# Performance work log

Measured on AMD Instinct MI355X. Metric: run time of the kernel, lower is better.

## Reference

```python
import jax, jax.numpy as jnp
import numpy as np

B, S, H = 4, 2048, 1024

def setup_inputs() -> dict:
    key = jax.random.key(0)
    ks = jax.random.split(key, 4)
    scale = 1.0 / np.sqrt(H)
    x = jax.random.normal(ks[0], (B, S, H), dtype=jnp.float32)
    Wq = jax.random.normal(ks[1], (H, H), dtype=jnp.float32) * scale
    Wk = jax.random.normal(ks[2], (H, H), dtype=jnp.float32) * scale
    Wv = jax.random.normal(ks[3], (H, H), dtype=jnp.float32) * scale
    bq = jnp.zeros((H,), dtype=jnp.float32)
    bk = jnp.zeros((H,), dtype=jnp.float32)
    bv = jnp.zeros((H,), dtype=jnp.float32)
    return {"x": x, "Wq": Wq, "bq": bq, "Wk": Wk, "bk": bk, "Wv": Wv, "bv": bv}

def reference(x, Wq, bq, Wk, bk, Wv, bv):
    # Linear: y = x @ W^T + b (torch nn.Linear convention)
    Q = jnp.einsum('bsh,oh->bso', x, Wq) + bq
    K = jnp.einsum('bsh,oh->bso', x, Wk) + bk
    V = jnp.einsum('bsh,oh->bso', x, Wv) + bv
    scores = jnp.einsum('bqh,bkh->bqk', Q, K) / jnp.sqrt(jnp.float32(H))
    attn = jax.nn.softmax(scores, axis=-1)
    return jnp.einsum('bqk,bkh->bqh', attn, V)
```

## Files before the change

### kernel.cpp

```cpp
#include <hip/hip_runtime.h>
#include <cstdint>
#include <cstddef>


typedef __bf16 bf16;
typedef _Float16 f16;
typedef __bf16 bf16x8 __attribute__((ext_vector_type(8)));
typedef __bf16 bf16x4 __attribute__((ext_vector_type(4)));
typedef _Float16 f16x8 __attribute__((ext_vector_type(8)));
typedef float f32x4 __attribute__((ext_vector_type(4)));

#define BM 256
#define BKT 64
#define LDS_TOTAL 131072

#define XQ (8388608 / 4)
#define WQ (1048576 / 4)
__global__ __launch_bounds__(256)
void cvt_all(const float* __restrict__ x, const float* __restrict__ Wq,
             const float* __restrict__ Wk, const float* __restrict__ Wv,
             bf16* __restrict__ xb, bf16* __restrict__ Wqkv)
{
    const int i = blockIdx.x * 256 + threadIdx.x;
    const float* src;
    bf16* dst;
    if (i < XQ) {
        src = x + 4 * (size_t)i;
        dst = xb + 4 * (size_t)i;
    } else {
        const int j = i - XQ;
        const int w = j / WQ;
        const int off = j - w * WQ;
        const float* ws_ = (w == 0) ? Wq : (w == 1) ? Wk : Wv;
        src = ws_ + 4 * (size_t)off;
        dst = Wqkv + 4 * (size_t)j;
    }
    f32x4 v = *(const f32x4*)src;
    bf16x4 o;
#pragma unroll
    for (int r = 0; r < 4; ++r) o[r] = (bf16)v[r];
    *(bf16x4*)dst = o;
}

template <int OUTMODE, int NW_N>
__global__ __launch_bounds__(512, 2)
void gemm256(const bf16* __restrict__ A, const bf16* __restrict__ Bm,
             const float* __restrict__ bias0, const float* __restrict__ bias1,
             const float* __restrict__ bias2, void* __restrict__ C,
             int K, int N, float alpha, long zA, long zB, long zC)
{
    constexpr int MI = 2 * NW_N;
    extern __shared__ __align__(16) char smem[];
    auto lds3 = (__attribute__((address_space(3))) char*)smem;

    const int tid  = threadIdx.x;
    const int lane = tid & 63;
    const int wid  = tid >> 6;
    const int quad = lane >> 4;
    const int l16  = lane & 15;
    const int wc   = (wid % NW_N) * 64;
    const int wr   = (wid / NW_N) * (MI * 16);

    const unsigned gx = gridDim.x, gy = gridDim.y;
    unsigned flat = blockIdx.x + gx * (blockIdx.y + gy * blockIdx.z);
    const unsigned chunk = (gx * gy * gridDim.z) >> 3;
    flat = (flat & 7u) * chunk + (flat >> 3);
    const int bx = flat % gx;
    const unsigned r2 = flat / gx;
    const int by = r2 % gy;
    const int z  = r2 / gy;

    const int m0 = by * BM;
    const int n0 = bx * (NW_N * 64);

    const bf16* Ab = A + (size_t)z * zA + (size_t)m0 * K;
    const bf16* Bb = Bm + (size_t)z * zB + (size_t)n0 * K;

    const int sr  = tid >> 3;
    const int sc  = (tid & 7) ^ (sr & 7);
    const size_t soff = (size_t)sr * K + (size_t)sc * 8;
    const long  hstep = 64L * K;
    const long  h1off = 128L * K;
    const unsigned dmabase = (unsigned)(wid * 1024);

#define STAGE(g, ldsoff)                                                       \
    do {                                                                       \
        __builtin_amdgcn_global_load_lds(                                      \
            (const __attribute__((address_space(1))) void*)((g) + soff),       \
            (__attribute__((address_space(3))) void*)(lds3 + (ldsoff) + dmabase), \
            16, 0, 0);                                                         \
        __builtin_amdgcn_global_load_lds(                                      \
            (const __attribute__((address_space(1))) void*)((g) + soff + hstep), \
            (__attribute__((address_space(3))) void*)(lds3 + (ldsoff) + 8192 + dmabase), \
            16, 0, 0);                                                         \
    } while (0)

    const char* pa = (const char*)smem + (wr + l16) * 128;
    const int x0 = (quad ^ (l16 & 7)) * 16;

    const int NT = K / BKT;
    f32x4 acc[MI][4] = {};

    if constexpr (NW_N == 4) {
        const char* pb = (const char*)smem + 65536 + (wc + l16) * 128;
        bf16x8 af[4][2], b01[2][2], b23[2][2];

        STAGE(Ab, 0u);           STAGE(Ab + h1off, 16384u);
        STAGE(Bb, 65536u);       STAGE(Bb + h1off, 65536u + 16384u);
        STAGE(Ab + 64, 32768u);  STAGE(Ab + 64 + h1off, 32768u + 16384u);
        asm volatile("s_waitcnt vmcnt(4)\n\ts_barrier" ::: "memory");

        for (int t = 0; t < NT; ++t) {
            const unsigned d  = (unsigned)(t & 1) * 32768u;
            const unsigned dn = 32768u - d;
            const char* paT = pa + d;
            const char* pbT = pb + d;

#pragma unroll
            for (int i = 0; i < 4; ++i) {
                af[i][0] = *(const bf16x8*)(paT + i * 2048 + x0);
                af[i][1] = *(const bf16x8*)(paT + i * 2048 + (x0 ^ 64));
            }
#pragma unroll
            for (int j = 0; j < 2; ++j) {
                b01[j][0] = *(const bf16x8*)(pbT + j * 2048 + x0);
                b01[j][1] = *(const bf16x8*)(pbT + j * 2048 + (x0 ^ 64));
            }
            if (t + 1 < NT) STAGE(Bb + (t + 1) * 64, 65536u + dn);
            __builtin_amdgcn_s_setprio(1);
#pragma unroll
            for (int i = 0; i < 4; ++i)
#pragma unroll
                for (int j = 0; j < 2; ++j) {
                    acc[i][j] = __builtin_amdgcn_mfma_f32_16x16x32_bf16(
                        af[i][0], b01[j][0], acc[i][j], 0, 0, 0);
                    acc[i][j] = __builtin_amdgcn_mfma_f32_16x16x32_bf16(
                        af[i][1], b01[j][1], acc[i][j], 0, 0, 0);
                }
            __builtin_amdgcn_s_setprio(0);

#pragma unroll
            for (int j = 0; j < 2; ++j) {
                b23[j][0] = *(const bf16x8*)(pbT + (2 + j) * 2048 + x0);
                b23[j][1] = *(const bf16x8*)(pbT + (2 + j) * 2048 + (x0 ^ 64));
            }
            if (t + 1 < NT) STAGE(Bb + (t + 1) * 64 + h1off, 65536u + dn + 16384u);
            __builtin_amdgcn_s_setprio(1);
#pragma unroll
            for (int i = 0; i < 4; ++i)
#pragma unroll
                for (int j = 0; j < 2; ++j) {
                    acc[i][2 + j] = __builtin_amdgcn_mfma_f32_16x16x32_bf16(
                        af[i][0], b23[j][0], acc[i][2 + j], 0, 0, 0);
                    acc[i][2 + j] = __builtin_amdgcn_mfma_f32_16x16x32_bf16(
                        af[i][1], b23[j][1], acc[i][2 + j], 0, 0, 0);
                }
            __builtin_amdgcn_s_setprio(0);

#pragma unroll
            for (int i = 0; i < 4; ++i) {
                af[i][0] = *(const bf16x8*)(paT + (4 + i) * 2048 + x0);
                af[i][1] = *(const bf16x8*)(paT + (4 + i) * 2048 + (x0 ^ 64));
            }
            __builtin_amdgcn_s_setprio(1);
#pragma unroll
            for (int i = 0; i < 4; ++i)
#pragma unroll
                for (int j = 0; j < 2; ++j) {
                    acc[4 + i][2 + j] = __builtin_amdgcn_mfma_f32_16x16x32_bf16(
                        af[i][0], b23[j][0], acc[4 + i][2 + j], 0, 0, 0);
                    acc[4 + i][2 + j] = __builtin_amdgcn_mfma_f32_16x16x32_bf16(
                        af[i][1], b23[j][1], acc[4 + i][2 + j], 0, 0, 0);
                }
            __builtin_amdgcn_s_setprio(0);

            asm volatile("s_barrier" ::: "memory");

#pragma unroll
            for (int j = 0; j < 2; ++j) {
                b01[j][0] = *(const bf16x8*)(pbT + j * 2048 + x0);
                b01[j][1] = *(const bf16x8*)(pbT + j * 2048 + (x0 ^ 64));
            }
            if (t + 2 < NT) {
                STAGE(Ab + (t + 2) * 64, d);
                STAGE(Ab + (t + 2) * 64 + h1off, d + 16384u);
            }
            __builtin_amdgcn_s_setprio(1);
#pragma unroll
            for (int i = 0; i < 4; ++i)
#pragma unroll
                for (int j = 0; j < 2; ++j) {
                    acc[4 + i][j] = __builtin_amdgcn_mfma_f32_16x16x32_bf16(
                        af[i][0], b01[j][0], acc[4 + i][j], 0, 0, 0);
                    acc[4 + i][j] = __builtin_amdgcn_mfma_f32_16x16x32_bf16(
                        af[i][1], b01[j][1], acc[4 + i][j], 0, 0, 0);
                }
            __builtin_amdgcn_s_setprio(0);

            if (t + 2 < NT)
                asm volatile("s_waitcnt vmcnt(4)\n\ts_barrier" ::: "memory");
            else if (t + 1 < NT)
                asm volatile("s_waitcnt vmcnt(0)\n\ts_barrier" ::: "memory");
        }
    } else {
        bf16x8 af[2][2], bfr[4][2];

        STAGE(Ab, 0u);           STAGE(Ab + h1off, 16384u);
        STAGE(Bb, 98304u);
        STAGE(Ab + 64, 32768u);  STAGE(Ab + 64 + h1off, 32768u + 16384u);
        asm volatile("s_waitcnt vmcnt(4)\n\ts_barrier" ::: "memory");

        for (int t = 0; t < NT; ++t) {
            const char* paT = pa + (unsigned)(t % 3) * 32768u;
            const char* pbT = (const char*)smem + 98304u +
                              (unsigned)(t & 1) * 16384u + (wc + l16) * 128;

#pragma unroll
            for (int i = 0; i < 2; ++i) {
                af[i][0] = *(const bf16x8*)(paT + i * 2048 + x0);
                af[i][1] = *(const bf16x8*)(paT + i * 2048 + (x0 ^ 64));
            }
#pragma unroll
            for (int j = 0; j < 4; ++j) {
                bfr[j][0] = *(const bf16x8*)(pbT + j * 2048 + x0);
                bfr[j][1] = *(const bf16x8*)(pbT + j * 2048 + (x0 ^ 64));
            }
            if (t + 1 < NT)
                STAGE(Bb + (t + 1) * 64, 98304u + (unsigned)((t + 1) & 1) * 16384u);
            __builtin_amdgcn_s_setprio(1);
#pragma unroll
            for (int i = 0; i < 2; ++i)
#pragma unroll
                for (int j = 0; j < 4; ++j) {
                    acc[i][j] = __builtin_amdgcn_mfma_f32_16x16x32_bf16(
                        af[i][0], bfr[j][0], acc[i][j], 0, 0, 0);
                    acc[i][j] = __builtin_amdgcn_mfma_f32_16x16x32_bf16(
                        af[i][1], bfr[j][1], acc[i][j], 0, 0, 0);
                }
            __builtin_amdgcn_s_setprio(0);

#pragma unroll
            for (int i = 0; i < 2; ++i) {
                af[i][0] = *(const bf16x8*)(paT + (2 + i) * 2048 + x0);
                af[i][1] = *(const bf16x8*)(paT + (2 + i) * 2048 + (x0 ^ 64));
            }
            if (t + 2 < NT) {
                const unsigned da = (unsigned)((t + 2) % 3) * 32768u;
                STAGE(Ab + (t + 2) * 64, da);
                STAGE(Ab + (t + 2) * 64 + h1off, da + 16384u);
            }
            __builtin_amdgcn_s_setprio(1);
#pragma unroll
            for (int i = 0; i < 2; ++i)
#pragma unroll
                for (int j = 0; j < 4; ++j) {
                    acc[2 + i][j] = __builtin_amdgcn_mfma_f32_16x16x32_bf16(
                        af[i][0], bfr[j][0], acc[2 + i][j], 0, 0, 0);
                    acc[2 + i][j] = __builtin_amdgcn_mfma_f32_16x16x32_bf16(
                        af[i][1], bfr[j][1], acc[2 + i][j], 0, 0, 0);
                }
            __builtin_amdgcn_s_setprio(0);

            if (t + 2 < NT)
                asm volatile("s_waitcnt vmcnt(4)\n\ts_barrier" ::: "memory");
            else if (t + 1 < NT)
                asm volatile("s_waitcnt vmcnt(0)\n\ts_barrier" ::: "memory");
        }
    }
#undef STAGE

#pragma unroll
    for (int j = 0; j < 4; ++j) {
        const int col3 = n0 + wc + j * 16 + l16;
#pragma unroll
        for (int i = 0; i < MI; ++i) {
            const int rbase = m0 + wr + i * 16 + quad * 4;
            if (OUTMODE == 2) {
                f16* Cf = (f16*)C + (size_t)z * zC;
#pragma unroll
                for (int r = 0; r < 4; ++r)
                    Cf[(size_t)(rbase + r) * N + col3] = (f16)(acc[i][j][r] * alpha);
            } else if (OUTMODE == 3) {
                float* Cf = (float*)C + (size_t)z * zC;
#pragma unroll
                for (int r = 0; r < 4; ++r)
                    Cf[(size_t)(rbase + r) * N + col3] = acc[i][j][r];
            } else {
                const int mat = col3 >> 10;
                const int col = col3 & 1023;
                const float* bp = (mat == 0) ? bias0 : (mat == 1) ? bias1 : bias2;
                const float bj = bp[col];
                if (mat < 2) {
                    bf16* Cb = (bf16*)C + (size_t)mat * (8u << 20);
#pragma unroll
                    for (int r = 0; r < 4; ++r)
                        Cb[(size_t)(rbase + r) * 1024 + col] =
                            (bf16)(acc[i][j][r] + bj);
                } else {
                    bf16* Cb = (bf16*)C + (size_t)(16u << 20);
                    const int b = rbase >> 11;
                    const int s = rbase & 2047;
                    bf16x4 tmp;
#pragma unroll
                    for (int r = 0; r < 4; ++r) tmp[r] = (bf16)(acc[i][j][r] + bj);
                    *(bf16x4*)(Cb + (((size_t)((b << 10) + col)) << 11) + s) = tmp;
                }
            }
        }
    }
}

__device__ __forceinline__ float wred_max(float v)
{
#pragma unroll
    for (int o = 32; o > 0; o >>= 1) v = fmaxf(v, __shfl_xor(v, o, 64));
    return v;
}
__device__ __forceinline__ float wred_sum(float v)
{
#pragma unroll
    for (int o = 32; o > 0; o >>= 1) v += __shfl_xor(v, o, 64);
    return v;
}

__global__ __launch_bounds__(256)
void softmax_rows(const f16* __restrict__ Sc, bf16* __restrict__ P)
{
    constexpr int NC = 2048;
    const size_t row = blockIdx.x;
    const f16* src = Sc + row * NC;
    bf16* dst = P + row * NC;
    const int tid = threadIdx.x;

    f16x8 in = *(const f16x8*)(src + tid * 8);
    float v[8];
    float m = -3.4e38f;
#pragma unroll
    for (int i = 0; i < 8; ++i) {
        v[i] = (float)in[i];
        m = fmaxf(m, v[i]);
    }
    m = wred_max(m);

    __shared__ float redm[4], reds[4];
    if ((tid & 63) == 0) redm[tid >> 6] = m;
    __syncthreads();
    m = fmaxf(fmaxf(redm[0], redm[1]), fmaxf(redm[2], redm[3]));

    float s = 0.f;
#pragma unroll
    for (int i = 0; i < 8; ++i) { v[i] = __expf(v[i] - m); s += v[i]; }
    s = wred_sum(s);
    if ((tid & 63) == 0) reds[tid >> 6] = s;
    __syncthreads();
    s = reds[0] + reds[1] + reds[2] + reds[3];

    const float inv = 1.f / s;
    bf16x8 o;
#pragma unroll
    for (int i = 0; i < 8; ++i) o[i] = (bf16)(v[i] * inv);
    *(bf16x8*)(dst + tid * 8) = o;
}

extern "C" void kernel_launch(void* const* d_in, const int* in_sizes, int n_in,
                              void* d_out, int out_size, void* d_ws, size_t ws_size,
                              hipStream_t stream)
{
    constexpr int B = 4, S = 2048, H = 1024;
    const float* x  = (const float*)d_in[0];
    const float* Wq = (const float*)d_in[1];
    const float* bq = (const float*)d_in[2];
    const float* Wk = (const float*)d_in[3];
    const float* bk = (const float*)d_in[4];
    const float* Wv = (const float*)d_in[5];
    const float* bv = (const float*)d_in[6];
    float* out = (float*)d_out;

    char* ws = (char*)d_ws;
    bf16* xb   = (bf16*)ws;
    bf16* Wqkv = (bf16*)(ws + (size_t)(16 << 20));
    bf16* Q    = (bf16*)(ws + (size_t)(22 << 20));
    bf16* Kp   = (bf16*)(ws + (size_t)(38 << 20));
    bf16* Vt   = (bf16*)(ws + (size_t)(54 << 20));
    f16*  Sc   = (f16*) (ws + (size_t)(70 << 20));
    bf16* P    = (bf16*)(ws + (size_t)(22 << 20));

    static bool attr_done = false;
    if (!attr_done) {
        attr_done = true;
        (void)hipFuncSetAttribute(reinterpret_cast<const void*>(gemm256<4, 4>),
                                  hipFuncAttributeMaxDynamicSharedMemorySize,
                                  LDS_TOTAL);
        (void)hipFuncSetAttribute(reinterpret_cast<const void*>(gemm256<2, 4>),
                                  hipFuncAttributeMaxDynamicSharedMemorySize,
                                  LDS_TOTAL);
        (void)hipFuncSetAttribute(reinterpret_cast<const void*>(gemm256<3, 2>),
                                  hipFuncAttributeMaxDynamicSharedMemorySize,
                                  LDS_TOTAL);
    }

    dim3 blk(256, 1, 1);
    dim3 blk512(512, 1, 1);

    cvt_all<<<dim3((XQ + 3 * WQ) / 256), blk, 0, stream>>>(
        x, Wq, Wk, Wv, xb, Wqkv);

    gemm256<4, 4><<<dim3(3 * H / 256, (B * S) / BM, 1), blk512, LDS_TOTAL, stream>>>(
        xb, Wqkv, bq, bk, bv, Q, H, 3 * H, 1.0f, 0, 0, 0);

    gemm256<2, 4><<<dim3(S / 256, S / BM, B), blk512, LDS_TOTAL, stream>>>(
        Q, Kp, nullptr, nullptr, nullptr, Sc, H, S, 0.03125f,
        (long)S * H, (long)S * H, (long)S * S);

    softmax_rows<<<dim3(B * S), blk, 0, stream>>>(Sc, P);

    gemm256<3, 2><<<dim3(H / 128, S / BM, B), blk512, LDS_TOTAL, stream>>>(
        P, Vt, nullptr, nullptr, nullptr, out, S, H, 1.0f,
        (long)S * S, (long)H * S, (long)S * H);
}
```

Before: 248.5 us.

## Replace QKV projection GEMM with simpler 128x128 double-buffered kernel

The fused QKV projection moves from the hand-pipelined 256-row, 512-thread gemm256 kernel to a new 256-thread gemm_bt kernel. The new kernel uses 128x128 tiles, static LDS double buffering and a plain syncthreads schedule. This gives the projection four times as many blocks, which may improve CU occupancy and load balance on a 8192x3072 output. The cost is less data reuse per tile and a simpler pipeline that may hide memory latency less well than the tuned original. gemm256 is trimmed to the attention-only output modes.

Result: no change. 245.3 us (-1.3%).

```diff
diff --git a/kernel.cpp b/kernel.cpp
--- a/kernel.cpp
+++ b/kernel.cpp
@@ -10,8 +10,6 @@
 typedef _Float16 f16x8 __attribute__((ext_vector_type(8)));
 typedef float f32x4 __attribute__((ext_vector_type(4)));
 
-#define BM 256
-#define BKT 64
 #define LDS_TOTAL 131072
 
 #define XQ (8388608 / 4)
@@ -42,11 +40,137 @@
     *(bf16x4*)dst = o;
 }
 
+#define BM1 128
+#define BN1 128
+#define BK1 64
+
+__device__ __forceinline__ void stage_tile(const bf16* __restrict__ g, int ld,
+                                           bf16* lds_generic, int tid)
+{
+    auto lds3 = (__attribute__((address_space(3))) char*)lds_generic;
+    const int wave = tid >> 6;
+#pragma unroll
+    for (int issue = 0; issue < 4; ++issue) {
+        const int p   = issue * 256 + tid;
+        const int row = p >> 3;
+        const int cp  = p & 7;
+        const int c   = cp ^ (row & 7);
+        const bf16* gp = g + (size_t)row * ld + c * 8;
+        const unsigned wave_base = (unsigned)(issue * 4096 + wave * 1024);
+        __builtin_amdgcn_global_load_lds(
+            (const __attribute__((address_space(1))) void*)gp,
+            (__attribute__((address_space(3))) void*)(lds3 + wave_base),
+            16, 0, 0);
+    }
+}
+
+__device__ __forceinline__ bf16x8 read_frag(const bf16* lds, int row, int chunk)
+{
+    const int cp = chunk ^ (row & 7);
+    return *(const bf16x8*)(lds + row * BK1 + cp * 8);
+}
+
+template <int OUTMODE, int DBUF>
+__global__ __launch_bounds__(256, DBUF ? 2 : 4)
+void gemm_bt(const bf16* __restrict__ A, const bf16* __restrict__ Bm,
+             const float* __restrict__ bias0, const float* __restrict__ bias1,
+             const float* __restrict__ bias2, void* __restrict__ C,
+             int K, int N, float alpha, long zA, long zB, long zC)
+{
+    __shared__ alignas(16) bf16 As[DBUF + 1][BM1 * BK1];
+    __shared__ alignas(16) bf16 Bs[DBUF + 1][BN1 * BK1];
+
+    const int tid  = threadIdx.x;
+    const int lane = tid & 63;
+    const int wid  = tid >> 6;
+    const int wr   = (wid >> 1) * 64;
+    const int wc   = (wid & 1) * 64;
+    const int quad = lane >> 4;
+    const int l16  = lane & 15;
+
+    const int m0 = blockIdx.y * BM1;
+    const int n0 = blockIdx.x * BN1;
+    const int z  = blockIdx.z;
+
+    const bf16* Ab = A + (size_t)z * zA + (size_t)m0 * K;
+    const bf16* Bb = Bm + (size_t)z * zB + (size_t)n0 * K;
+
+    f32x4 acc[4][4] = {};
+
+    if (DBUF) {
+        stage_tile(Ab, K, As[0], tid);
+        stage_tile(Bb, K, Bs[0], tid);
+    }
+
+    const int niter = K / BK1;
+    for (int it = 0; it < niter; ++it) {
+        int cur;
+        if (DBUF) {
+            cur = it & 1;
+            __syncthreads();
+            if (it + 1 < niter) {
+                stage_tile(Ab + (it + 1) * BK1, K, As[cur ^ 1], tid);
+                stage_tile(Bb + (it + 1) * BK1, K, Bs[cur ^ 1], tid);
+            }
+        } else {
+            cur = 0;
+            __syncthreads();
+            stage_tile(Ab + it * BK1, K, As[0], tid);
+            stage_tile(Bb + it * BK1, K, Bs[0], tid);
+            __syncthreads();
+        }
+#pragma unroll
+        for (int h = 0; h < 2; ++h) {
+            bf16x8 af[4], bfr[4];
+#pragma unroll
+            for (int i = 0; i < 4; ++i)
+                af[i]  = read_frag(As[cur], wr + i * 16 + l16, h * 4 + quad);
+#pragma unroll
+            for (int j = 0; j < 4; ++j)
+                bfr[j] = read_frag(Bs[cur], wc + j * 16 + l16, h * 4 + quad);
+
+#pragma unroll
+            for (int i = 0; i < 4; ++i)
+#pragma unroll
+                for (int j = 0; j < 4; ++j)
+                    acc[i][j] = __builtin_amdgcn_mfma_f32_16x16x32_bf16(
+                        af[i], bfr[j], acc[i][j], 0, 0, 0);
+        }
+    }
+
+#pragma unroll
+    for (int j = 0; j < 4; ++j) {
+        const int col3 = n0 + wc + j * 16 + l16;
+#pragma unroll
+        for (int i = 0; i < 4; ++i) {
+            const int rbase = m0 + wr + i * 16 + quad * 4;
+            const int mat = col3 >> 10;
+            const int col = col3 & 1023;
+            const float* bp = (mat == 0) ? bias0 : (mat == 1) ? bias1 : bias2;
+            const float bj = bp[col];
+            if (mat < 2) {
+                bf16* Cb = (bf16*)C + (size_t)mat * (8u << 20);
+#pragma unroll
+                for (int r = 0; r < 4; ++r)
+                    Cb[(size_t)(rbase + r) * 1024 + col] =
+                        (bf16)(acc[i][j][r] + bj);
+            } else {
+                bf16* Cb = (bf16*)C + (size_t)(16u << 20);
+                const int b = rbase >> 11;
+                const int s = rbase & 2047;
+                bf16x4 tmp;
+#pragma unroll
+                for (int r = 0; r < 4; ++r) tmp[r] = (bf16)(acc[i][j][r] + bj);
+                *(bf16x4*)(Cb + (((size_t)((b << 10) + col)) << 11) + s) = tmp;
+            }
+        }
+    }
+}
+
 template <int OUTMODE, int NW_N>
 __global__ __launch_bounds__(512, 2)
 void gemm256(const bf16* __restrict__ A, const bf16* __restrict__ Bm,
-             const float* __restrict__ bias0, const float* __restrict__ bias1,
-             const float* __restrict__ bias2, void* __restrict__ C,
+             void* __restrict__ C,
              int K, int N, float alpha, long zA, long zB, long zC)
 {
     constexpr int MI = 2 * NW_N;
@@ -70,7 +194,7 @@
     const int by = r2 % gy;
     const int z  = r2 / gy;
 
-    const int m0 = by * BM;
+    const int m0 = by * 256;
     const int n0 = bx * (NW_N * 64);
 
     const bf16* Ab = A + (size_t)z * zA + (size_t)m0 * K;
@@ -98,7 +222,7 @@
     const char* pa = (const char*)smem + (wr + l16) * 128;
     const int x0 = (quad ^ (l16 & 7)) * 16;
 
-    const int NT = K / BKT;
+    const int NT = K / 64;
     f32x4 acc[MI][4] = {};
 
     if constexpr (NW_N == 4) {
@@ -280,31 +404,11 @@
 #pragma unroll
                 for (int r = 0; r < 4; ++r)
                     Cf[(size_t)(rbase + r) * N + col3] = (f16)(acc[i][j][r] * alpha);
-            } else if (OUTMODE == 3) {
+            } else {
                 float* Cf = (float*)C + (size_t)z * zC;
 #pragma unroll
                 for (int r = 0; r < 4; ++r)
                     Cf[(size_t)(rbase + r) * N + col3] = acc[i][j][r];
-            } else {
-                const int mat = col3 >> 10;
-                const int col = col3 & 1023;
-                const float* bp = (mat == 0) ? bias0 : (mat == 1) ? bias1 : bias2;
-                const float bj = bp[col];
-                if (mat < 2) {
-                    bf16* Cb = (bf16*)C + (size_t)mat * (8u << 20);
-#pragma unroll
-                    for (int r = 0; r < 4; ++r)
-                        Cb[(size_t)(rbase + r) * 1024 + col] =
-                            (bf16)(acc[i][j][r] + bj);
-                } else {
-                    bf16* Cb = (bf16*)C + (size_t)(16u << 20);
-                    const int b = rbase >> 11;
-                    const int s = rbase & 2047;
-                    bf16x4 tmp;
-#pragma unroll
-                    for (int r = 0; r < 4; ++r) tmp[r] = (bf16)(acc[i][j][r] + bj);
-                    *(bf16x4*)(Cb + (((size_t)((b << 10) + col)) << 11) + s) = tmp;
-                }
             }
         }
     }
@@ -388,9 +492,6 @@
     static bool attr_done = false;
     if (!attr_done) {
         attr_done = true;
-        (void)hipFuncSetAttribute(reinterpret_cast<const void*>(gemm256<4, 4>),
-                                  hipFuncAttributeMaxDynamicSharedMemorySize,
-                                  LDS_TOTAL);
         (void)hipFuncSetAttribute(reinterpret_cast<const void*>(gemm256<2, 4>),
                                   hipFuncAttributeMaxDynamicSharedMemorySize,
                                   LDS_TOTAL);
@@ -405,16 +506,16 @@
     cvt_all<<<dim3((XQ + 3 * WQ) / 256), blk, 0, stream>>>(
         x, Wq, Wk, Wv, xb, Wqkv);
 
-    gemm256<4, 4><<<dim3(3 * H / 256, (B * S) / BM, 1), blk512, LDS_TOTAL, stream>>>(
+    gemm_bt<4, 1><<<dim3(3 * H / BN1, (B * S) / BM1, 1), blk, 0, stream>>>(
         xb, Wqkv, bq, bk, bv, Q, H, 3 * H, 1.0f, 0, 0, 0);
 
-    gemm256<2, 4><<<dim3(S / 256, S / BM, B), blk512, LDS_TOTAL, stream>>>(
-        Q, Kp, nullptr, nullptr, nullptr, Sc, H, S, 0.03125f,
+    gemm256<2, 4><<<dim3(S / 256, S / 256, B), blk512, LDS_TOTAL, stream>>>(
+        Q, Kp, Sc, H, S, 0.03125f,
         (long)S * H, (long)S * H, (long)S * S);
 
     softmax_rows<<<dim3(B * S), blk, 0, stream>>>(Sc, P);
 
-    gemm256<3, 2><<<dim3(H / 128, S / BM, B), blk512, LDS_TOTAL, stream>>>(
-        P, Vt, nullptr, nullptr, nullptr, out, S, H, 1.0f,
+    gemm256<3, 2><<<dim3(H / 128, S / 256, B), blk512, LDS_TOTAL, stream>>>(
+        P, Vt, out, S, H, 1.0f,
         (long)S * S, (long)H * S, (long)S * H);
 }
```
